# Kernel tuning notes

Measured on AMD Instinct MI355X. Metric: run time of the kernel, lower is better.

Reference implementation:

```python
import jax, jax.numpy as jnp
import numpy as np

NUM_HEADS = 16
HEAD_DIM = 128
HIDDEN = NUM_HEADS * HEAD_DIM  # 2048
ROPE_BASE = 10000.0


def _rope_tables(seq_len, dtype=jnp.float32):
    inv_freq = 1.0 / (ROPE_BASE ** (jnp.arange(0, HEAD_DIM, 2, dtype=jnp.float32) / HEAD_DIM))
    freqs = jnp.arange(seq_len, dtype=jnp.float32)[:, None] * inv_freq[None, :]  # [S, hd/2]
    return jnp.cos(freqs).astype(dtype), jnp.sin(freqs).astype(dtype)


def _apply_rope(x, cos, sin):
    # x: [B, S, H, hd]; interleaved even/odd rotation
    B, S, H, D = x.shape
    xr = x.reshape(B, S, H, D // 2, 2)
    x_even, x_odd = xr[..., 0], xr[..., 1]
    c = cos[None, :, None, :]
    s = sin[None, :, None, :]
    rot_even = x_even * c - x_odd * s
    rot_odd = x_even * s + x_odd * c
    return jnp.stack([rot_even, rot_odd], axis=-1).reshape(B, S, H, D)


def setup_inputs() -> dict:
    key = jax.random.key(0)
    k1, k2, k3, k4, k5 = jax.random.split(key, 5)
    B, S = 2, 2048
    hidden_states = jax.random.normal(k1, (B, S, HIDDEN), dtype=jnp.float32)
    attention_mask = jnp.zeros((B, 1, 1, S), dtype=jnp.float32)
    scale = 1.0 / np.sqrt(HIDDEN)
    Wqkv = jax.random.normal(k2, (3 * HIDDEN, HIDDEN), dtype=jnp.float32) * scale
    bqkv = jnp.zeros((3 * HIDDEN,), dtype=jnp.float32)
    Wout = jax.random.normal(k3, (HIDDEN, HIDDEN), dtype=jnp.float32) * scale
    bout = jnp.zeros((HIDDEN,), dtype=jnp.float32)
    return {"hidden_states": hidden_states, "attention_mask": attention_mask,
            "Wqkv": Wqkv, "bqkv": bqkv, "Wout": Wout, "bout": bout}


def reference(hidden_states, attention_mask, Wqkv, bqkv, Wout, bout):
    B, S, _ = hidden_states.shape
    scale = 1.0 / np.sqrt(HEAD_DIM)
    qkv = hidden_states @ Wqkv.T + bqkv                      # [B, S, 3*HIDDEN]
    qkv = qkv.reshape(B, S, 3, NUM_HEADS, HEAD_DIM)
    q, k, v = qkv[:, :, 0], qkv[:, :, 1], qkv[:, :, 2]       # [B, S, H, hd]
    cos, sin = _rope_tables(S, hidden_states.dtype)
    q = _apply_rope(q, cos, sin)
    k = _apply_rope(k, cos, sin)
    scores = jnp.einsum('bqhd,bkhd->bhqk', q, k) * scale     # [B, H, S, S]
    scores = scores + attention_mask
    probs = jax.nn.softmax(scores, axis=-1)
    ctx = jnp.einsum('bhqk,bkhd->bqhd', probs, v)            # [B, S, H, hd]
    ctx = ctx.reshape(B, S, HIDDEN)
    return ctx @ Wout.T + bout
```

## Files before the change

kernel.cpp:

```cpp
#include <hip/hip_runtime.h>
#include <math.h>

#define HID    2048
#define NH     16
#define HD     128
#define SEQ    2048
#define NBATCH 2

typedef __attribute__((ext_vector_type(8))) short bf16x8;
typedef __attribute__((ext_vector_type(4))) float f32x4;

__device__ __forceinline__ short f2bf(float f) {
    union { float f; unsigned u; } x; x.f = f;
    unsigned r = x.u + 0x7fffu + ((x.u >> 16) & 1u);
    return (short)(r >> 16);
}
__device__ __forceinline__ float bf2f(short s) {
    union { unsigned u; float f; } y;
    y.u = ((unsigned)(unsigned short)s) << 16;
    return y.f;
}

__device__ __forceinline__ void gl_lds16(const short* g, short* l) {
    __builtin_amdgcn_global_load_lds(
        (const __attribute__((address_space(1))) unsigned int*)g,
        (__attribute__((address_space(3))) unsigned int*)l, 16, 0, 0);
}

__global__ __launch_bounds__(256) void rope_table_kernel(float* __restrict__ ct,
                                                         float* __restrict__ st) {
    int idx = blockIdx.x * 256 + threadIdx.x;
    if (idx >= SEQ * 64) return;
    int s = idx >> 6;
    int i = idx & 63;
    double inv = pow(10000.0, -(double)i / 64.0);
    float freq = (float)s * (float)inv;
    ct[idx] = cosf(freq);
    st[idx] = sinf(freq);
}

__global__ __launch_bounds__(256) void split_h_kernel(const float* __restrict__ in,
                                                      short* __restrict__ oh, int n4) {
    int i = blockIdx.x * 256 + threadIdx.x;
    if (i >= n4) return;
    float4 v = ((const float4*)in)[i];
    short4 h;
    h.x = f2bf(v.x); h.y = f2bf(v.y); h.z = f2bf(v.z); h.w = f2bf(v.w);
    *(short4*)(oh + 4 * (size_t)i) = h;
}

#define LDSA 0
#define LDSB 4096

template <int MODE>
__global__ __launch_bounds__(256, 3) void gemm_bf16_kernel(
    const short* __restrict__ Ah, const short* __restrict__ Bh,
    const float* __restrict__ bias, float* __restrict__ C,
    short* __restrict__ qb, short* __restrict__ kbf, short* __restrict__ vTt,
    const float* __restrict__ ct, const float* __restrict__ st) {
    __shared__ short lds[MODE == 0 ? 18432 : 8192];

    const int t     = threadIdx.x;
    const int w     = t >> 6;
    const int lane  = t & 63;
    const int mfrag = lane & 15;
    const int quad  = lane >> 4;
    const int wm    = (w >> 1) * 64;
    const int wn    = (w & 1) * 64;
    const int m0    = blockIdx.y * 128;
    const int n0    = blockIdx.x * 128;

    const int srow   = lane >> 2;
    const int schunk = (((lane & 3) ^ ((lane >> 3) & 3))) * 8;
    const short* gA0 = Ah + (size_t)(m0 + w * 16 + srow) * HID + schunk;
    const short* gA1 = Ah + (size_t)(m0 + 64 + w * 16 + srow) * HID + schunk;
    const short* gB0 = Bh + (size_t)(n0 + w * 16 + srow) * HID + schunk;
    const short* gB1 = Bh + (size_t)(n0 + 64 + w * 16 + srow) * HID + schunk;
    short* lA0 = &lds[LDSA + (w * 16) * 32];
    short* lA1 = &lds[LDSA + (64 + w * 16) * 32];
    short* lB0 = &lds[LDSB + (w * 16) * 32];
    short* lB1 = &lds[LDSB + (64 + w * 16) * 32];

    const int chA = 8 * (quad ^ ((mfrag >> 1) & 3));

    f32x4 acc[4][4];
#pragma unroll
    for (int i = 0; i < 4; ++i)
#pragma unroll
        for (int j = 0; j < 4; ++j) acc[i][j] = (f32x4){0.f, 0.f, 0.f, 0.f};

    for (int kt = 0; kt < HID; kt += 32) {
        __syncthreads();
        gl_lds16(gA0 + kt, lA0);
        gl_lds16(gA1 + kt, lA1);
        gl_lds16(gB0 + kt, lB0);
        gl_lds16(gB1 + kt, lB1);
        __syncthreads();

        bf16x8 ah[4], bh[4];
#pragma unroll
        for (int mt = 0; mt < 4; ++mt)
            ah[mt] = *(const bf16x8*)&lds[LDSA + (wm + mt * 16 + mfrag) * 32 + chA];
#pragma unroll
        for (int nt = 0; nt < 4; ++nt)
            bh[nt] = *(const bf16x8*)&lds[LDSB + (wn + nt * 16 + mfrag) * 32 + chA];

#pragma unroll
        for (int mt = 0; mt < 4; ++mt)
#pragma unroll
            for (int nt = 0; nt < 4; ++nt)
                acc[mt][nt] = __builtin_amdgcn_mfma_f32_16x16x32_bf16(
                    ah[mt], bh[nt], acc[mt][nt], 0, 0, 0);
    }

    float bcol[4];
#pragma unroll
    for (int nt = 0; nt < 4; ++nt) bcol[nt] = bias[n0 + wn + nt * 16 + mfrag];

    if (MODE == 0) {
        const int which = n0 >> 11;
        const int h     = (n0 & 2047) >> 7;
        const int bidx  = m0 >> 11;
        if (which < 2) {
            short* dst = (which == 0) ? qb : kbf;
            const float post = (which == 0) ? 0.08838834764831845f : 1.0f;
#pragma unroll
            for (int mt = 0; mt < 4; ++mt)
#pragma unroll
                for (int r = 0; r < 4; ++r) {
                    int sl = (m0 & 2047) + wm + mt * 16 + 4 * quad + r;
#pragma unroll
                    for (int nt = 0; nt < 4; ++nt) {
                        float x  = acc[mt][nt][r] + bcol[nt];
                        float px = __shfl_xor(x, 1, 64);
                        int   d  = wn + nt * 16 + mfrag;
                        float c  = ct[sl * 64 + (d >> 1)];
                        float sn = st[sl * 64 + (d >> 1)];
                        float rot = (mfrag & 1) ? fmaf(px, sn, x * c)
                                                : (x * c - px * sn);
                        dst[((size_t)(bidx * NH + h) * SEQ + sl) * HD + d] =
                            f2bf(rot * post);
                    }
                }
        } else {
            __syncthreads();
            short* tw = &lds[w * 4608];
#pragma unroll
            for (int mt = 0; mt < 4; ++mt)
#pragma unroll
                for (int nt = 0; nt < 4; ++nt)
#pragma unroll
                    for (int r = 0; r < 4; ++r)
                        tw[(nt * 16 + mfrag) * 72 + (mt * 16 + 4 * quad + r)] =
                            f2bf(acc[mt][nt][r] + bcol[nt]);
            const size_t vbase = (size_t)(bidx * NH + h) * HD * SEQ;
            const int sbase = (m0 & 2047) + wm;
#pragma unroll
            for (int it = 0; it < 8; ++it) {
                int dl  = it * 8 + (lane >> 3);
                int cch = (lane & 7) ^ (lane >> 3);
                bf16x8 row = *(const bf16x8*)&tw[dl * 72 + cch * 8];
                *(bf16x8*)(vTt + vbase + (size_t)(wn + dl) * SEQ + sbase + cch * 8) = row;
            }
        }
    } else {
#pragma unroll
        for (int mt = 0; mt < 4; ++mt)
#pragma unroll
            for (int r = 0; r < 4; ++r) {
                int m = m0 + wm + mt * 16 + 4 * quad + r;
#pragma unroll
                for (int nt = 0; nt < 4; ++nt)
                    C[(size_t)m * HID + n0 + wn + nt * 16 + mfrag] =
                        acc[mt][nt][r] + bcol[nt];
            }
    }
}

#define LDSK 0
#define LDSV 8192
#define LDSP 16384

__global__ __launch_bounds__(512, 4) void attn_mfma_kernel(
    const short* __restrict__ qb, const short* __restrict__ kbf,
    const short* __restrict__ vTt, const float* __restrict__ mask,
    short* __restrict__ ctxb) {
    __shared__ __align__(16) short lds[25600];

    const int t    = threadIdx.x;
    const int w    = t >> 6;
    const int lane = t & 63;
    const int m    = lane & 15;
    const int quad = lane >> 4;

    const int id  = blockIdx.x;
    const int j   = id >> 3;
    const int bh  = (id & 7) * 4 + (j >> 4);
    const int q0  = (j & 15) * 128;
    const int b   = bh >> 4;
    const int h   = bh & 15;

    const size_t base = (size_t)bh * SEQ * HD;
    const short* kp = kbf + base;
    const short* vp = vTt + base;
    const float* mrow = mask + (size_t)b * SEQ;

    size_t kOff[2], vOff[2];
    short *ldsK[2], *ldsV[2];
#pragma unroll
    for (int u = 0; u < 2; ++u) {
        int rk = w * 8 + u * 4 + (lane >> 4);
        int ck = (lane & 15) ^ (rk & 7);
        kOff[u] = (size_t)rk * HD + ck * 8;
        ldsK[u] = &lds[LDSK + (w * 8 + u * 4) * 128];
        int rv = w * 16 + u * 8 + (lane >> 3);
        int cv = (lane & 7) ^ (rv & 7);
        vOff[u] = (size_t)rv * SEQ + cv * 8;
        ldsV[u] = &lds[LDSV + (w * 16 + u * 8) * 64];
    }

    const int srow = q0 + w * 16 + m;
    bf16x8 qh[4];
    {
        const short* qhp = qb + base + (size_t)srow * HD;
#pragma unroll
        for (int c = 0; c < 4; ++c)
            qh[c] = *(const bf16x8*)(qhp + 32 * c + 8 * quad);
    }

    f32x4 O[8];
    float m_i[4], l_i[4];
#pragma unroll
    for (int c = 0; c < 8; ++c) O[c] = (f32x4){0.f, 0.f, 0.f, 0.f};
#pragma unroll
    for (int r = 0; r < 4; ++r) { m_i[r] = -INFINITY; l_i[r] = 0.f; }

    const int sw = m & 7;

    for (int kt = 0; kt < SEQ / 64; ++kt) {
        const int k0 = kt * 64;

        __syncthreads();
#pragma unroll
        for (int u = 0; u < 2; ++u) {
            gl_lds16(kp + (size_t)k0 * HD + kOff[u], ldsK[u]);
            gl_lds16(vp + k0 + vOff[u], ldsV[u]);
        }
        __syncthreads();

        float mk[4];
#pragma unroll
        for (int c2 = 0; c2 < 4; ++c2) mk[c2] = mrow[k0 + 16 * c2 + m];

        f32x4 S[4];
#pragma unroll
        for (int c2 = 0; c2 < 4; ++c2) {
            f32x4 acc = (f32x4){0.f, 0.f, 0.f, 0.f};
#pragma unroll
            for (int c = 0; c < 4; ++c) {
                int pk = (4 * c + quad) ^ sw;
                bf16x8 kf = *(const bf16x8*)&lds[LDSK + (16 * c2 + m) * 128 + pk * 8];
                acc = __builtin_amdgcn_mfma_f32_16x16x32_bf16(qh[c], kf, acc, 0, 0, 0);
            }
            S[c2] = acc;
        }

        float alpha[4], p[4][4];
#pragma unroll
        for (int r = 0; r < 4; ++r) {
            float s0 = S[0][r] + mk[0];
            float s1 = S[1][r] + mk[1];
            float s2 = S[2][r] + mk[2];
            float s3 = S[3][r] + mk[3];
            float rm = fmaxf(fmaxf(s0, s1), fmaxf(s2, s3));
#pragma unroll
            for (int off = 1; off < 16; off <<= 1)
                rm = fmaxf(rm, __shfl_xor(rm, off, 64));
            float mn = fmaxf(m_i[r], rm);
            alpha[r] = __expf(m_i[r] - mn);
            p[0][r] = __expf(s0 - mn);
            p[1][r] = __expf(s1 - mn);
            p[2][r] = __expf(s2 - mn);
            p[3][r] = __expf(s3 - mn);
            float ts = (p[0][r] + p[1][r]) + (p[2][r] + p[3][r]);
#pragma unroll
            for (int off = 1; off < 16; off <<= 1)
                ts += __shfl_xor(ts, off, 64);
            l_i[r] = l_i[r] * alpha[r] + ts;
            m_i[r] = mn;
        }

#pragma unroll
        for (int c2 = 0; c2 < 4; ++c2)
#pragma unroll
            for (int r = 0; r < 4; ++r)
                lds[LDSP + w * 1152 + (4 * quad + r) * 72 + 16 * c2 + m] =
                    f2bf(p[c2][r]);

#pragma unroll
        for (int c = 0; c < 8; ++c)
#pragma unroll
            for (int r = 0; r < 4; ++r) O[c][r] *= alpha[r];

#pragma unroll
        for (int cc = 0; cc < 2; ++cc) {
            bf16x8 pf = *(const bf16x8*)&lds[LDSP + w * 1152 + m * 72 +
                                             32 * cc + 8 * quad];
#pragma unroll
            for (int c = 0; c < 8; ++c) {
                int pv = (4 * cc + quad) ^ sw;
                bf16x8 vf = *(const bf16x8*)&lds[LDSV + (16 * c + m) * 64 + pv * 8];
                O[c] = __builtin_amdgcn_mfma_f32_16x16x32_bf16(pf, vf, O[c], 0, 0, 0);
            }
        }
    }

#pragma unroll
    for (int r = 0; r < 4; ++r) {
        float inv = 1.0f / l_i[r];
        int s = q0 + w * 16 + 4 * quad + r;
        size_t off = ((size_t)(b * SEQ + s)) * HID + h * HD;
#pragma unroll
        for (int c = 0; c < 8; ++c)
            ctxb[off + 16 * c + m] = f2bf(O[c][r] * inv);
    }
}

extern "C" void kernel_launch(void* const* d_in, const int* in_sizes, int n_in,
                              void* d_out, int out_size, void* d_ws, size_t ws_size,
                              hipStream_t stream) {
    const float* hs   = (const float*)d_in[0];
    const float* mask = (const float*)d_in[1];
    const float* Wqkv = (const float*)d_in[2];
    const float* bqkv = (const float*)d_in[3];
    const float* Wout = (const float*)d_in[4];
    const float* bout = (const float*)d_in[5];
    float* out = (float*)d_out;

    const size_t qkv_elems = (size_t)NBATCH * NH * SEQ * HD;
    char* p = (char*)d_ws;
    float* cos_t = (float*)p; p += (size_t)SEQ * 64 * 4;
    float* sin_t = (float*)p; p += (size_t)SEQ * 64 * 4;
    short* qbf   = (short*)p; p += qkv_elems * 2;
    short* kbf   = (short*)p; p += qkv_elems * 2;
    short* vTt   = (short*)p; p += qkv_elems * 2;
    short* Wqkvh = (short*)p; p += (size_t)3 * HID * HID * 2;
    short* Wouth = (short*)p; p += (size_t)HID * HID * 2;
    short* Ahs   = (short*)p; p += qkv_elems * 2;
    short* ctxb  = Ahs;

    rope_table_kernel<<<(SEQ * 64 + 255) / 256, 256, 0, stream>>>(cos_t, sin_t);

    split_h_kernel<<<(int)(qkv_elems / 4 / 256), 256, 0, stream>>>(
        hs, Ahs, (int)(qkv_elems / 4));
    split_h_kernel<<<(int)((size_t)3 * HID * HID / 4 / 256), 256, 0, stream>>>(
        Wqkv, Wqkvh, (int)((size_t)3 * HID * HID / 4));
    split_h_kernel<<<(int)((size_t)HID * HID / 4 / 256), 256, 0, stream>>>(
        Wout, Wouth, (int)((size_t)HID * HID / 4));

    gemm_bf16_kernel<0><<<dim3(48, 32), 256, 0, stream>>>(
        Ahs, Wqkvh, bqkv, nullptr, qbf, kbf, vTt, cos_t, sin_t);

    attn_mfma_kernel<<<512, 512, 0, stream>>>(qbf, kbf, vTt, mask, ctxb);

    gemm_bf16_kernel<1><<<dim3(16, 32), 256, 0, stream>>>(
        ctxb, Wouth, bout, out, nullptr, nullptr, nullptr, nullptr, nullptr);
}
```

Measured before the change: 451.7 us.

## Double-buffer K/V tiles and add lazy softmax rescaling in attention kernel

The attention kernel now double-buffers K and V tiles in LDS, prefetching the next tile with global_load_lds while the current one is computed, which removes one barrier per iteration. It also skips the online-softmax rescale unless the row max grows by more than a threshold, and defers the row-sum reduction to the end. P is packed with v_cvt_pk_bf16_f32 into a swizzled LDS layout, and s_setprio is raised around the MFMA sections. LDS use grows from about 50KB to 80KB per block, which may cut occupancy below the launch-bound target of 4. The lazy rescale also relies on exp values staying bounded within the threshold.

Result: faster. 423.7 us (-6.2%).

```diff
diff --git a/kernel.cpp b/kernel.cpp
--- a/kernel.cpp
+++ b/kernel.cpp
@@ -6,6 +6,7 @@
 #define HD     128
 #define SEQ    2048
 #define NBATCH 2
+#define NT     (SEQ / 64)
 
 typedef __attribute__((ext_vector_type(8))) short bf16x8;
 typedef __attribute__((ext_vector_type(4))) float f32x4;
@@ -177,15 +178,17 @@
     }
 }
 
-#define LDSK 0
-#define LDSV 8192
-#define LDSP 16384
+#define AK0 0
+#define AK1 8192
+#define AV0 16384
+#define AV1 24576
+#define AP  32768
 
 __global__ __launch_bounds__(512, 4) void attn_mfma_kernel(
     const short* __restrict__ qb, const short* __restrict__ kbf,
     const short* __restrict__ vTt, const float* __restrict__ mask,
     short* __restrict__ ctxb) {
-    __shared__ __align__(16) short lds[25600];
+    __shared__ __align__(16) short lds[40960];
 
     const int t    = threadIdx.x;
     const int w    = t >> 6;
@@ -206,17 +209,17 @@
     const float* mrow = mask + (size_t)b * SEQ;
 
     size_t kOff[2], vOff[2];
-    short *ldsK[2], *ldsV[2];
+    int kDst[2], vDst[2];
 #pragma unroll
     for (int u = 0; u < 2; ++u) {
         int rk = w * 8 + u * 4 + (lane >> 4);
         int ck = (lane & 15) ^ (rk & 7);
         kOff[u] = (size_t)rk * HD + ck * 8;
-        ldsK[u] = &lds[LDSK + (w * 8 + u * 4) * 128];
+        kDst[u] = (w * 8 + u * 4) * 128;
         int rv = w * 16 + u * 8 + (lane >> 3);
         int cv = (lane & 7) ^ (rv & 7);
         vOff[u] = (size_t)rv * SEQ + cv * 8;
-        ldsV[u] = &lds[LDSV + (w * 16 + u * 8) * 64];
+        vDst[u] = (w * 16 + u * 8) * 64;
     }
 
     const int srow = q0 + w * 16 + m;
@@ -229,100 +232,139 @@
     }
 
     f32x4 O[8];
-    float m_i[4], l_i[4];
+    float m_i[4], l_p[4];
 #pragma unroll
     for (int c = 0; c < 8; ++c) O[c] = (f32x4){0.f, 0.f, 0.f, 0.f};
 #pragma unroll
-    for (int r = 0; r < 4; ++r) { m_i[r] = -INFINITY; l_i[r] = 0.f; }
+    for (int r = 0; r < 4; ++r) { m_i[r] = -INFINITY; l_p[r] = 0.f; }
 
     const int sw = m & 7;
-
-    for (int kt = 0; kt < SEQ / 64; ++kt) {
-        const int k0 = kt * 64;
+    const int pb = AP + w * 1024;
+    const int kcb = (m >> 3);
+    const int ml  = m & 7;
+
+#pragma unroll
+    for (int u = 0; u < 2; ++u) {
+        gl_lds16(kp + kOff[u], &lds[AK0 + kDst[u]]);
+        gl_lds16(vp + vOff[u], &lds[AV0 + vDst[u]]);
+    }
+
+    for (int kt = 0; kt < NT; ++kt) {
+        const int cur = kt & 1;
+        const int k0  = kt * 64;
 
         __syncthreads();
-#pragma unroll
-        for (int u = 0; u < 2; ++u) {
-            gl_lds16(kp + (size_t)k0 * HD + kOff[u], ldsK[u]);
-            gl_lds16(vp + k0 + vOff[u], ldsV[u]);
-        }
-        __syncthreads();
+
+        if (kt + 1 < NT) {
+            const int nk0 = (kt + 1) * 64;
+            const int nb  = cur ^ 1;
+#pragma unroll
+            for (int u = 0; u < 2; ++u) {
+                gl_lds16(kp + (size_t)nk0 * HD + kOff[u],
+                         &lds[(nb ? AK1 : AK0) + kDst[u]]);
+                gl_lds16(vp + nk0 + vOff[u],
+                         &lds[(nb ? AV1 : AV0) + vDst[u]]);
+            }
+        }
+
+        const short* kb = &lds[cur ? AK1 : AK0];
+        const short* vb = &lds[cur ? AV1 : AV0];
 
         float mk[4];
 #pragma unroll
         for (int c2 = 0; c2 < 4; ++c2) mk[c2] = mrow[k0 + 16 * c2 + m];
 
         f32x4 S[4];
+        __builtin_amdgcn_s_setprio(1);
 #pragma unroll
         for (int c2 = 0; c2 < 4; ++c2) {
             f32x4 acc = (f32x4){0.f, 0.f, 0.f, 0.f};
 #pragma unroll
             for (int c = 0; c < 4; ++c) {
                 int pk = (4 * c + quad) ^ sw;
-                bf16x8 kf = *(const bf16x8*)&lds[LDSK + (16 * c2 + m) * 128 + pk * 8];
+                bf16x8 kf = *(const bf16x8*)&kb[(16 * c2 + m) * 128 + pk * 8];
                 acc = __builtin_amdgcn_mfma_f32_16x16x32_bf16(qh[c], kf, acc, 0, 0, 0);
             }
             S[c2] = acc;
         }
-
-        float alpha[4], p[4][4];
+        __builtin_amdgcn_s_setprio(0);
+
+        float rm4[4];
 #pragma unroll
         for (int r = 0; r < 4; ++r) {
             float s0 = S[0][r] + mk[0];
             float s1 = S[1][r] + mk[1];
             float s2 = S[2][r] + mk[2];
             float s3 = S[3][r] + mk[3];
+            S[0][r] = s0; S[1][r] = s1; S[2][r] = s2; S[3][r] = s3;
             float rm = fmaxf(fmaxf(s0, s1), fmaxf(s2, s3));
 #pragma unroll
             for (int off = 1; off < 16; off <<= 1)
                 rm = fmaxf(rm, __shfl_xor(rm, off, 64));
-            float mn = fmaxf(m_i[r], rm);
-            alpha[r] = __expf(m_i[r] - mn);
-            p[0][r] = __expf(s0 - mn);
-            p[1][r] = __expf(s1 - mn);
-            p[2][r] = __expf(s2 - mn);
-            p[3][r] = __expf(s3 - mn);
-            float ts = (p[0][r] + p[1][r]) + (p[2][r] + p[3][r]);
-#pragma unroll
-            for (int off = 1; off < 16; off <<= 1)
-                ts += __shfl_xor(ts, off, 64);
-            l_i[r] = l_i[r] * alpha[r] + ts;
-            m_i[r] = mn;
-        }
-
-#pragma unroll
-        for (int c2 = 0; c2 < 4; ++c2)
-#pragma unroll
-            for (int r = 0; r < 4; ++r)
-                lds[LDSP + w * 1152 + (4 * quad + r) * 72 + 16 * c2 + m] =
-                    f2bf(p[c2][r]);
-
+            rm4[r] = rm;
+        }
+        int needI = (rm4[0] > m_i[0] + 8.f) | (rm4[1] > m_i[1] + 8.f) |
+                    (rm4[2] > m_i[2] + 8.f) | (rm4[3] > m_i[3] + 8.f);
+        if (__any(needI)) {
+#pragma unroll
+            for (int r = 0; r < 4; ++r) {
+                float mn = fmaxf(m_i[r], rm4[r]);
+                float a  = __expf(m_i[r] - mn);
+                m_i[r]   = mn;
+                l_p[r]  *= a;
+#pragma unroll
+                for (int c = 0; c < 8; ++c) O[c][r] *= a;
+            }
+        }
+        float p[4][4];
+#pragma unroll
+        for (int r = 0; r < 4; ++r) {
+#pragma unroll
+            for (int c2 = 0; c2 < 4; ++c2) p[c2][r] = __expf(S[c2][r] - m_i[r]);
+            l_p[r] += (p[0][r] + p[1][r]) + (p[2][r] + p[3][r]);
+        }
+
+#pragma unroll
+        for (int c2 = 0; c2 < 4; ++c2) {
+#pragma unroll
+            for (int jj = 0; jj < 2; ++jj) {
+                unsigned pkw;
+                asm("v_cvt_pk_bf16_f32 %0, %1, %2"
+                    : "=v"(pkw) : "v"(p[c2][2 * jj]), "v"(p[c2][2 * jj + 1]));
+                int ql = 4 * quad + 2 * jj;
+                int qh2 = ql + 1;
+                lds[pb + ql * 64 + (((2 * c2 + kcb) ^ (ql & 7)) << 3) + ml] =
+                    (short)(pkw & 0xffffu);
+                lds[pb + qh2 * 64 + (((2 * c2 + kcb) ^ (qh2 & 7)) << 3) + ml] =
+                    (short)(pkw >> 16);
+            }
+        }
+
+        __builtin_amdgcn_s_setprio(1);
+#pragma unroll
+        for (int cc = 0; cc < 2; ++cc) {
+            int pv = (4 * cc + quad) ^ sw;
+            bf16x8 pf = *(const bf16x8*)&lds[pb + m * 64 + (pv << 3)];
+#pragma unroll
+            for (int c = 0; c < 8; ++c) {
+                bf16x8 vf = *(const bf16x8*)&vb[(16 * c + m) * 64 + pv * 8];
+                O[c] = __builtin_amdgcn_mfma_f32_16x16x32_bf16(pf, vf, O[c], 0, 0, 0);
+            }
+        }
+        __builtin_amdgcn_s_setprio(0);
+    }
+
+#pragma unroll
+    for (int r = 0; r < 4; ++r) {
+        float lv = l_p[r];
+#pragma unroll
+        for (int off = 1; off < 16; off <<= 1) lv += __shfl_xor(lv, off, 64);
+        float inv = 1.0f / lv;
+        int s = q0 + w * 16 + 4 * quad + r;
+        size_t off2 = ((size_t)(b * SEQ + s)) * HID + h * HD;
 #pragma unroll
         for (int c = 0; c < 8; ++c)
-#pragma unroll
-            for (int r = 0; r < 4; ++r) O[c][r] *= alpha[r];
-
-#pragma unroll
-        for (int cc = 0; cc < 2; ++cc) {
-            bf16x8 pf = *(const bf16x8*)&lds[LDSP + w * 1152 + m * 72 +
-                                             32 * cc + 8 * quad];
-#pragma unroll
-            for (int c = 0; c < 8; ++c) {
-                int pv = (4 * cc + quad) ^ sw;
-                bf16x8 vf = *(const bf16x8*)&lds[LDSV + (16 * c + m) * 64 + pv * 8];
-                O[c] = __builtin_amdgcn_mfma_f32_16x16x32_bf16(pf, vf, O[c], 0, 0, 0);
-            }
-        }
-    }
-
-#pragma unroll
-    for (int r = 0; r < 4; ++r) {
-        float inv = 1.0f / l_i[r];
-        int s = q0 + w * 16 + 4 * quad + r;
-        size_t off = ((size_t)(b * SEQ + s)) * HID + h * HD;
-#pragma unroll
-        for (int c = 0; c < 8; ++c)
-            ctxb[off + 16 * c + m] = f2bf(O[c][r] * inv);
+            ctxb[off2 + 16 * c + m] = f2bf(O[c][r] * inv);
     }
 }
 
```
